# Kernel optimization log

Measured on AMD Instinct MI355X. Metric: run time of the kernel, lower is better.

The kernel has to match this reference:

```python
import jax, jax.numpy as jnp
import numpy as np

NPX = 128      # nPxPup
FOV = 512      # fovInPixel = 2*samp*nPxPup, samp=2
NMODES = 54    # len(jModes)
BATCH = 8
ALPHA = np.pi / 2


def _make_consts():
    # circular pupil on the nPxPup grid
    x = np.linspace(-1.0, 1.0, NPX)
    X, Y = np.meshgrid(x, x)
    pupil = ((X ** 2 + Y ** 2) <= 1.0).astype(np.float32)
    # 4-faced pyramid phase mask on the FOV grid, pre-fftshifted
    f = np.arange(FOV) - FOV / 2
    FX, FY = np.meshgrid(f, f)
    pyr_phase = ALPHA * (np.abs(FX) + np.abs(FY))
    pyr_mask = np.fft.fftshift(np.exp(-1j * pyr_phase)).astype(np.complex64)
    return pupil, pyr_mask


def setup_inputs() -> dict:
    key = jax.random.key(0)
    k1, k2 = jax.random.split(key)
    pupil_np, mask_np = _make_consts()
    pupil = jnp.asarray(pupil_np)                      # [NPX,NPX] float32
    pyrMask = jnp.asarray(mask_np)                     # [FOV,FOV] complex64 (fftshifted)
    # Zernike-like mode basis restricted to the pupil, column-major modes as in the torch buffer
    modes = jax.random.normal(k1, (NPX * NPX, NMODES), dtype=jnp.float32) * pupil.reshape(-1, 1)
    OL1 = (jnp.eye(NMODES, dtype=jnp.float32) * 0.1)   # learnable parameter
    inputs = jax.random.normal(k2, (BATCH, 1, NPX, NPX), dtype=jnp.float32) * pupil
    return {"inputs": inputs, "modes": modes, "OL1": OL1, "pupil": pupil, "pyrMask": pyrMask}


def _prop(phase, pupil, pyrMask):
    """Vanilla pyramid WFS propagation (modulation=0).
    phase: [B,1,NPX,NPX] -> intensity [B,1,FOV,FOV]."""
    u = (pupil * jnp.exp(1j * phase)).astype(jnp.complex64)
    npv = (FOV - NPX) // 2
    field = jnp.zeros(phase.shape[:2] + (FOV, FOV), dtype=jnp.complex64)
    field = field.at[:, :, npv:npv + NPX, npv:npv + NPX].set(u)
    buf = jnp.fft.fft2(field) * pyrMask          # focal plane * pyramid mask
    return jnp.abs(jnp.fft.fft2(buf)) ** 2       # detector intensity


def reference(inputs, modes, OL1, pupil, pyrMask):
    n_modes = OL1.shape[0]
    optModes = modes @ OL1                                     # [NPX*NPX, M]
    # reference (flat wavefront) intensity
    flat = (jnp.ones((NPX, NPX), jnp.float32) * (pupil > 0))[None, None]
    I0 = _prop(flat, pupil, pyrMask)
    I0 = I0 / jnp.sum(I0)                                      # [1,1,FOV,FOV]
    gainRow = jnp.sum(OL1, axis=1)                             # [M]
    # batch the per-mode +/- push-pull propagations in one FFT pass
    zim = optModes.T.reshape(n_modes, 1, NPX, NPX)
    phases = jnp.concatenate([zim, -zim], axis=0)              # [2M,1,NPX,NPX]
    I4 = _prop(phases, pupil, pyrMask)
    I4 = I4 / jnp.sum(I4, axis=(1, 2, 3), keepdims=True)
    sp = I4[:n_modes] - I0
    sm = I4[n_modes:] - I0
    MZc = 0.5 * (sp - sm) / gainRow[:, None, None, None]
    IM = MZc.reshape(n_modes, -1).T                            # [FOV*FOV, M]
    CM = jnp.linalg.pinv(IM)                                   # [M, FOV*FOV]
    # measurement
    Ip = _prop(inputs, pupil, pyrMask)                         # [B,1,FOV,FOV]
    Inorm = jnp.sum(Ip, axis=(1, 2, 3), keepdims=True)
    Ip = Ip / Inorm - I0
    y = CM @ Ip.reshape(Ip.shape[0], -1).T                     # [M, B]
    return y
```

## Files before the change

kernel.cpp:

```cpp
#include <hip/hip_runtime.h>
#include <math.h>

#define NPIXK 262144
#define ROWF2 584
#define ROWF2B 585

__device__ __forceinline__ int padi8(int i) { return i + (i >> 3); }
__device__ __forceinline__ int padi(int i) { return i + (i >> 5); }

#define WSYNC asm volatile("s_waitcnt lgkmcnt(0)" ::: "memory")
#define CFENCE asm volatile("" ::: "memory")

__device__ __forceinline__ float2 cmul(float2 a, float2 b) {
    return make_float2(a.x * b.x - a.y * b.y, a.x * b.y + a.y * b.x);
}

__device__ __forceinline__ void twchain(float ang, float2 tw[8]) {
    float s, c;
    sincosf(ang, &s, &c);
    float2 w1 = make_float2(c, s);
    float2 w2 = cmul(w1, w1);
    float2 w4 = cmul(w2, w2);
    tw[1] = w1;
    tw[2] = w2;
    tw[3] = cmul(w1, w2);
    tw[4] = w4;
    tw[5] = cmul(w1, w4);
    tw[6] = cmul(w2, w4);
    tw[7] = cmul(tw[3], w4);
}

__device__ __forceinline__ void fft8f(float vr[8], float vi[8]) {
    float er[4], ei[4], orr[4], oi[4];
    {
        float t0r = vr[0] + vr[4], t0i = vi[0] + vi[4];
        float t1r = vr[0] - vr[4], t1i = vi[0] - vi[4];
        float t2r = vr[2] + vr[6], t2i = vi[2] + vi[6];
        float t3r = vi[2] - vi[6], t3i = vr[6] - vr[2];
        er[0] = t0r + t2r; ei[0] = t0i + t2i;
        er[1] = t1r + t3r; ei[1] = t1i + t3i;
        er[2] = t0r - t2r; ei[2] = t0i - t2i;
        er[3] = t1r - t3r; ei[3] = t1i - t3i;
    }
    {
        float t0r = vr[1] + vr[5], t0i = vi[1] + vi[5];
        float t1r = vr[1] - vr[5], t1i = vi[1] - vi[5];
        float t2r = vr[3] + vr[7], t2i = vi[3] + vi[7];
        float t3r = vi[3] - vi[7], t3i = vr[7] - vr[3];
        orr[0] = t0r + t2r; oi[0] = t0i + t2i;
        orr[1] = t1r + t3r; oi[1] = t1i + t3i;
        orr[2] = t0r - t2r; oi[2] = t0i - t2i;
        orr[3] = t1r - t3r; oi[3] = t1i - t3i;
    }
    const float c = 0.70710678118654752440f;
    vr[0] = er[0] + orr[0]; vi[0] = ei[0] + oi[0];
    vr[4] = er[0] - orr[0]; vi[4] = ei[0] - oi[0];
    float t1r = c * (orr[1] + oi[1]), t1i = c * (oi[1] - orr[1]);
    vr[1] = er[1] + t1r; vi[1] = ei[1] + t1i;
    vr[5] = er[1] - t1r; vi[5] = ei[1] - t1i;
    float t2r = oi[2], t2i = -orr[2];
    vr[2] = er[2] + t2r; vi[2] = ei[2] + t2i;
    vr[6] = er[2] - t2r; vi[6] = ei[2] - t2i;
    float t3r = c * (oi[3] - orr[3]), t3i = -c * (orr[3] + oi[3]);
    vr[3] = er[3] + t3r; vi[3] = ei[3] + t3i;
    vr[7] = er[3] - t3r; vi[7] = ei[3] - t3i;
}

__device__ __forceinline__ void fft8_s34(float vr[8], float vi[8]) {
    const float c = 0.70710678118654752440f;
    float x3r = vr[3], x3i = vi[3], x4r = vr[4], x4i = vi[4];
    float A = c * (x3r + x3i), B = c * (x3r - x3i);
    vr[0] = x3r + x4r; vi[0] = x3i + x4i;
    vr[1] = -B - x4r;  vi[1] = -A - x4i;
    vr[2] = x4r - x3i; vi[2] = x3r + x4i;
    vr[3] = A - x4r;   vi[3] = -B - x4i;
    vr[4] = x4r - x3r; vi[4] = x4i - x3i;
    vr[5] = B - x4r;   vi[5] = A - x4i;
    vr[6] = x3i + x4r; vi[6] = x4i - x3r;
    vr[7] = -A - x4r;  vi[7] = B - x4i;
}

template <int SPARSE>
__device__ __forceinline__ void fft512v(float2* L, int t,
                                        float vr[8], float vi[8]) {
    if (SPARSE) fft8_s34(vr, vi); else fft8f(vr, vi);
    {
        float2* wb = L + 9 * t;
#pragma unroll
        for (int r = 0; r < 8; ++r) wb[r] = make_float2(vr[r], vi[r]);
    }
    float2 tw[8];
    twchain((float)(t & 7) * -0.09817477042468103870f, tw);
    WSYNC;
    {
        const float2* rb = L + t + (t >> 3);
        { float2 a = rb[0]; vr[0] = a.x; vi[0] = a.y; }
#pragma unroll
        for (int r = 1; r < 8; ++r) {
            float2 a = rb[72 * r];
            float2 w = tw[r];
            vr[r] = a.x * w.x - a.y * w.y;
            vi[r] = a.x * w.y + a.y * w.x;
        }
        fft8f(vr, vi);
        WSYNC;
        float2* wb = L + 9 * t;
#pragma unroll
        for (int r = 0; r < 8; ++r) wb[r] = make_float2(vr[r], vi[r]);
    }
    twchain((float)t * -0.01227184630308512985f, tw);
    WSYNC;
    {
        const float2* rb = L + 9 * (t & 7) + (t >> 3);
        { float2 a = rb[0]; vr[0] = a.x; vi[0] = a.y; }
#pragma unroll
        for (int r = 1; r < 8; ++r) {
            float2 a = rb[72 * r];
            float2 w = tw[r];
            vr[r] = a.x * w.x - a.y * w.y;
            vi[r] = a.x * w.y + a.y * w.x;
        }
        fft8f(vr, vi);
    }
}

template <int SPARSE>
__device__ __forceinline__ void fft512v2(float2* LA, float2* LB, int t,
                                         float avr[8], float avi[8],
                                         float bvr[8], float bvi[8]) {
    if (SPARSE) { fft8_s34(avr, avi); fft8_s34(bvr, bvi); }
    else        { fft8f(avr, avi);   fft8f(bvr, bvi); }
    {
        float2* wa = LA + 9 * t;
        float2* wb = LB + 9 * t;
#pragma unroll
        for (int r = 0; r < 8; ++r) wa[r] = make_float2(avr[r], avi[r]);
#pragma unroll
        for (int r = 0; r < 8; ++r) wb[r] = make_float2(bvr[r], bvi[r]);
    }
    float2 tw[8];
    twchain((float)(t & 7) * -0.09817477042468103870f, tw);
    WSYNC;
    {
        const float2* ra = LA + t + (t >> 3);
        const float2* rb = LB + t + (t >> 3);
        { float2 a = ra[0]; avr[0] = a.x; avi[0] = a.y; }
        { float2 b = rb[0]; bvr[0] = b.x; bvi[0] = b.y; }
#pragma unroll
        for (int r = 1; r < 8; ++r) {
            float2 a = ra[72 * r], b = rb[72 * r], w = tw[r];
            avr[r] = a.x * w.x - a.y * w.y;  avi[r] = a.x * w.y + a.y * w.x;
            bvr[r] = b.x * w.x - b.y * w.y;  bvi[r] = b.x * w.y + b.y * w.x;
        }
        fft8f(avr, avi); fft8f(bvr, bvi);
        WSYNC;
        float2* wa = LA + 9 * t;
        float2* wb = LB + 9 * t;
#pragma unroll
        for (int r = 0; r < 8; ++r) wa[r] = make_float2(avr[r], avi[r]);
#pragma unroll
        for (int r = 0; r < 8; ++r) wb[r] = make_float2(bvr[r], bvi[r]);
    }
    twchain((float)t * -0.01227184630308512985f, tw);
    WSYNC;
    {
        const float2* ra = LA + 9 * (t & 7) + (t >> 3);
        const float2* rb = LB + 9 * (t & 7) + (t >> 3);
        { float2 a = ra[0]; avr[0] = a.x; avi[0] = a.y; }
        { float2 b = rb[0]; bvr[0] = b.x; bvi[0] = b.y; }
#pragma unroll
        for (int r = 1; r < 8; ++r) {
            float2 a = ra[72 * r], b = rb[72 * r], w = tw[r];
            avr[r] = a.x * w.x - a.y * w.y;  avi[r] = a.x * w.y + a.y * w.x;
            bvr[r] = b.x * w.x - b.y * w.y;  bvi[r] = b.x * w.y + b.y * w.x;
        }
        fft8f(avr, avi); fft8f(bvr, bvi);
    }
}

#define FFT_LDS __shared__ float2 lds[4][ROWF2];

__device__ __forceinline__ double lsx(int i) {
    if (i == 127) return 1.0;
    return __dadd_rn(__dmul_rn((double)i, 2.0 / 127.0), -1.0);
}
__device__ __forceinline__ double pupilAt(int r, int c) {
    double xc = lsx(c), xr = lsx(r);
    double s = __dadd_rn(__dmul_rn(xc, xc), __dmul_rn(xr, xr));
    return (s <= 1.0) ? 1.0 : 0.0;
}

__global__ __launch_bounds__(256, 8) void k_s1(const float* __restrict__ optT,
                                               const float* __restrict__ inputs,
                                               float2* __restrict__ T1, int giBase) {
    FFT_LDS
    int tid = threadIdx.x, w = tid >> 6, t = tid & 63;
    int r = (blockIdx.x & 31) * 4 + w;
    int im = blockIdx.x >> 5;
    int gi;
    if (giBase >= 0)            gi = giBase + im;
    else if (giBase == -1)      gi = (im == 0) ? 0 : 108 + im;
    else                        gi = (im < 9) ? ((im == 0) ? 0 : 108 + im)
                                              : im - 8;

    float vr[8], vi[8];
#pragma unroll
    for (int q = 0; q < 8; ++q) { vr[q] = 0.f; vi[q] = 0.f; }
#pragma unroll
    for (int h = 0; h < 2; ++h) {
        int c = t + 64 * h;
        int p = r * 128 + c;
        float pu = (float)pupilAt(r, c);
        float ph;
        if (gi == 0) {
            ph = pu;
        } else if (gi < 109) {
            ph = optT[(gi - 1) * 16384 + p];
        } else {
            ph = inputs[(gi - 109) * 16384 + p];
        }
        float s, cs; sincosf(ph, &s, &cs);
        vr[3 + h] = pu * cs; vi[3 + h] = pu * s;
    }
    fft512v<1>(lds[w], t, vr, vi);
    WSYNC;
#pragma unroll
    for (int q = 0; q < 8; ++q) {
        int d = t + 64 * q;
        lds[w][padi8(d)] = make_float2(vr[q], vi[q]);
    }
    __syncthreads();
    int r0 = (blockIdx.x & 31) * 4;
    float2* dst = T1 + (size_t)im * 65536;
#pragma unroll
    for (int it = 0; it < 8; ++it) {
        int g = it * 256 + tid;
        int l = g >> 2, rr = g & 3;
        dst[(size_t)l * 128 + r0 + rr] = lds[rr][padi8(l)];
    }
}

__global__ __launch_bounds__(256, 4) void k_s23(const float2* __restrict__ T1,
                                                float2* __restrict__ C2p) {
    __shared__ float2 lds[8][ROWF2B];
    int tid = threadIdx.x, w = tid >> 6, t = tid & 63;
    int imgL = blockIdx.x >> 6;
    int l0 = (blockIdx.x & 63) * 8;
    int lA = l0 + w, lB = l0 + 4 + w;
    const float2* srcA = T1 + (size_t)imgL * 65536 + (size_t)lA * 128;
    const float2* srcB = T1 + (size_t)imgL * 65536 + (size_t)lB * 128;
    float avr[8], avi[8], bvr[8], bvi[8];
#pragma unroll
    for (int q = 0; q < 8; ++q) { avr[q] = 0.f; avi[q] = 0.f; bvr[q] = 0.f; bvi[q] = 0.f; }
    { float2 a0 = srcA[t], a1 = srcA[t + 64];
      avr[3] = a0.x; avi[3] = a0.y; avr[4] = a1.x; avi[4] = a1.y; }
    { float2 b0 = srcB[t], b1 = srcB[t + 64];
      bvr[3] = b0.x; bvi[3] = b0.y; bvr[4] = b1.x; bvi[4] = b1.y; }
    fft512v2<1>(lds[w], lds[w + 4], t, avr, avi, bvr, bvi);
    int glA = (lA <= 256) ? lA : 512 - lA;
    int glB = (lB <= 256) ? lB : 512 - lB;
#pragma unroll
    for (int q = 0; q < 8; ++q) {
        int k = t + 64 * q;
        int gk = (k <= 256) ? k : 512 - k;
        {   int n = (gk + glA) & 3;
            float a = avr[q], b = avi[q], X, Y;
            if (n == 0)      { X = a;  Y = b;  }
            else if (n == 1) { X = b;  Y = -a; }
            else if (n == 2) { X = -a; Y = -b; }
            else             { X = -b; Y = a;  }
            avr[q] = X; avi[q] = Y; }
        {   int n = (gk + glB) & 3;
            float a = bvr[q], b = bvi[q], X, Y;
            if (n == 0)      { X = a;  Y = b;  }
            else if (n == 1) { X = b;  Y = -a; }
            else if (n == 2) { X = -a; Y = -b; }
            else             { X = -b; Y = a;  }
            bvr[q] = X; bvi[q] = Y; }
    }
    fft512v2<0>(lds[w], lds[w + 4], t, avr, avi, bvr, bvi);
    WSYNC;
#pragma unroll
    for (int q = 0; q < 8; ++q) {
        int d = padi8(t + 64 * q);
        lds[w][d]     = make_float2(avr[q], avi[q]);
        lds[w + 4][d] = make_float2(bvr[q], bvi[q]);
    }
    __syncthreads();
    float2* dst = C2p + (size_t)imgL * NPIXK;
#pragma unroll
    for (int it = 0; it < 16; ++it) {
        int g = it * 256 + tid;
        int p = g >> 3, rr = g & 7;
        dst[(size_t)p * 512 + l0 + rr] = lds[rr][padi8(p)];
    }
}

__global__ __launch_bounds__(256, 8) void k_s4(const float2* __restrict__ C2,
                                               float* __restrict__ dst,
                                               const float* __restrict__ I0,
                                               int ep) {
    FFT_LDS
    int tid = threadIdx.x, w = tid >> 6, t = tid & 63;
    int imgL = blockIdx.x >> 7, p = (blockIdx.x & 127) * 4 + w;
    const float2* src = C2 + (size_t)imgL * NPIXK + (size_t)p * 512;
    float vr[8], vi[8];
#pragma unroll
    for (int q = 0; q < 8; ++q) { float2 a = src[t + 64 * q]; vr[q] = a.x; vi[q] = a.y; }
    fft512v<0>(lds[w], t, vr, vi);
    size_t rowOff = (size_t)p * 512;
    float* drow = dst + (size_t)imgL * NPIXK + rowOff;
    if (ep == 0) {
#pragma unroll
        for (int q = 0; q < 8; ++q) {
            int k = t + 64 * q;
            drow[k] = vr[q] * vr[q] + vi[q] * vi[q];
        }
    } else {
#pragma unroll
        for (int q = 0; q < 8; ++q) {
            int k = t + 64 * q;
            float mag2 = vr[q] * vr[q] + vi[q] * vi[q];
            drow[k] = mag2 - I0[rowOff + k];
        }
    }
}

__global__ __launch_bounds__(256, 8) void k_s4pm(const float2* __restrict__ C2p,
                                                 float* __restrict__ dst,
                                                 const double* __restrict__ gainInv,
                                                 int gBase) {
    FFT_LDS
    int tid = threadIdx.x, w = tid >> 6, t = tid & 63;
    int imgL = blockIdx.x >> 7, q2 = blockIdx.x & 127;
    int p = 2 * q2 + (w & 1) + (w >> 1) * 256;
    const float2* src = C2p + (size_t)imgL * NPIXK + (size_t)p * 512;
    float vr[8], vi[8], m2[8];
#pragma unroll
    for (int q = 0; q < 8; ++q) { float2 a = src[t + 64 * q]; vr[q] = a.x; vi[q] = a.y; }
    fft512v<0>(lds[w], t, vr, vi);
    WSYNC;
    float* mrow = (float*)lds[w];
#pragma unroll
    for (int q = 0; q < 8; ++q) {
        m2[q] = vr[q] * vr[q] + vi[q] * vi[q];
        mrow[padi(t + 64 * q)] = m2[q];
    }
    __syncthreads();
    float g = (float)gainInv[gBase + imgL];
    float* drow = dst + (size_t)imgL * NPIXK + (size_t)p * 512;
    const float* prow = (const float*)lds[w ^ 2];
#pragma unroll
    for (int q = 0; q < 8; ++q) {
        int qp = (q + 4) & 7;
        float other = prow[padi(t + 64 * qp)];
        drow[t + 64 * q] = g * (m2[q] - other);
    }
}

__global__ __launch_bounds__(256, 4) void k_s4x(const float2* __restrict__ C2p,
                                                float* __restrict__ I0buf,
                                                float* __restrict__ Mz,
                                                const double* __restrict__ gainInv) {
    __shared__ float2 lds[8][ROWF2B];
    int tid = threadIdx.x, w = tid >> 6, t = tid & 63;
    int im = blockIdx.x >> 6, b6 = blockIdx.x & 63;
    float avr[8], avi[8], bvr[8], bvi[8];
    if (im < 9) {
        int pA = b6 * 8 + w, pB = b6 * 8 + 4 + w;
        const float2* srcA = C2p + (size_t)im * NPIXK + (size_t)pA * 512;
        const float2* srcB = C2p + (size_t)im * NPIXK + (size_t)pB * 512;
#pragma unroll
        for (int q = 0; q < 8; ++q) {
            float2 a = srcA[t + 64 * q]; avr[q] = a.x; avi[q] = a.y;
            float2 b = srcB[t + 64 * q]; bvr[q] = b.x; bvi[q] = b.y;
        }
        fft512v2<0>(lds[w], lds[w + 4], t, avr, avi, bvr, bvi);
        float* dA = I0buf + (size_t)im * NPIXK + (size_t)pA * 512;
        float* dB = I0buf + (size_t)im * NPIXK + (size_t)pB * 512;
#pragma unroll
        for (int q = 0; q < 8; ++q) {
            int k = t + 64 * q;
            dA[k] = avr[q] * avr[q] + avi[q] * avi[q];
            dB[k] = bvr[q] * bvr[q] + bvi[q] * bvi[q];
        }
    } else {
        int mi = im - 9;
        int pA = b6 * 4 + w;
        int pB = pA + 256;
        const float2* srcA = C2p + (size_t)im * NPIXK + (size_t)pA * 512;
        const float2* srcB = C2p + (size_t)im * NPIXK + (size_t)pB * 512;
#pragma unroll
        for (int q = 0; q < 8; ++q) {
            float2 a = srcA[t + 64 * q]; avr[q] = a.x; avi[q] = a.y;
            float2 b = srcB[t + 64 * q]; bvr[q] = b.x; bvi[q] = b.y;
        }
        fft512v2<0>(lds[w], lds[w + 4], t, avr, avi, bvr, bvi);
        float m2A[8], m2B[8];
#pragma unroll
        for (int q = 0; q < 8; ++q) {
            m2A[q] = avr[q] * avr[q] + avi[q] * avi[q];
            m2B[q] = bvr[q] * bvr[q] + bvi[q] * bvi[q];
        }
        float g = (float)gainInv[mi];
        float* dA = Mz + (size_t)mi * NPIXK + (size_t)pA * 512;
        float* dB = Mz + (size_t)mi * NPIXK + (size_t)pB * 512;
#pragma unroll
        for (int q = 0; q < 8; ++q) {
            int k = t + 64 * q;
            int qp = (q + 4) & 7;
            dA[k] = g * (m2A[q] - m2B[qp]);
            dB[k] = g * (m2B[q] - m2A[qp]);
        }
    }
}

__global__ __launch_bounds__(256) void k_modes(const float* __restrict__ modes,
                                               const float* __restrict__ OL1,
                                               float* __restrict__ optT,
                                               double* __restrict__ gainInv,
                                               double* __restrict__ G,
                                               double* __restrict__ bmat) {
    __shared__ float sM[64 * 54];
    __shared__ float sOL[54 * 54];
    int tid = threadIdx.x;
    if (blockIdx.x == 0) {
        for (int i = tid; i < 54 * 54; i += 256) G[i] = 0.0;
        for (int i = tid; i < 54 * 8; i += 256) bmat[i] = 0.0;
    }
    for (int i = tid; i < 54 * 54; i += 256) sOL[i] = OL1[i];
    const float* msrc = modes + (size_t)blockIdx.x * 64 * 54;
    for (int i = tid; i < 64 * 54; i += 256) sM[i] = msrc[i];
    __syncthreads();
    int pl = tid & 63, mg = tid >> 6;
    int p = blockIdx.x * 64 + pl;
    const float* mrow = sM + pl * 54;
    for (int m = mg; m < 54; m += 4) {
        double acc = 0.0;
#pragma unroll
        for (int j = 0; j < 54; ++j)
            acc += (double)mrow[j] * (double)sOL[j * 54 + m];
        optT[(size_t)m * 16384 + p] = (float)acc;
    }
    if (blockIdx.x == 0 && tid < 54) {
        double g = 0.0;
        for (int j = 0; j < 54; ++j) g += (double)sOL[tid * 54 + j];
        gainInv[tid] = 0.5 / g;
    }
}

__device__ __forceinline__ float dot4(float4 a, float4 b) {
    return a.x * b.x + a.y * b.y + a.z * b.z + a.w * b.w;
}

#define GPROWS 2304
__global__ __launch_bounds__(256, 4) void k_gram54(const float* __restrict__ Mz,
                                                   const float* __restrict__ V,
                                                   const float* __restrict__ I0,
                                                   float* __restrict__ part,
                                                   int subI0) {
    __shared__ float Ms[64 * 128];
    int tid = threadIdx.x;
    int task = tid / 7, sl = tid - task * 7;
    if (task > 35) task = 35;
    int oi = 0, rem = task;
    while (rem >= 8 - oi) { rem -= 8 - oi; ++oi; }
    int oj = oi + rem;
    int ra = 8 * oi, rb = 8 * oj;
    int start = (32 * sl) / 7, len = (32 * (sl + 1)) / 7 - start;
    int rot = tid % len;
    float s[64];
#pragma unroll
    for (int q = 0; q < 64; ++q) s[q] = 0.f;

#pragma unroll 1
    for (int ch = 0; ch < 2; ++ch) {
        size_t P0 = ((size_t)blockIdx.x * 2 + ch) * 128;
        if (ch) __syncthreads();
        for (int idx = tid; idx < 64 * 32; idx += 256) {
            int i = idx >> 5, v4 = idx & 31;
            float4 vv;
            if (i < 54) {
                vv = *(const float4*)(Mz + (size_t)i * NPIXK + P0 + v4 * 4);
            } else if (i < 62) {
                vv = *(const float4*)(V + (size_t)(i - 54) * NPIXK + P0 + v4 * 4);
                if (subI0) {
                    float4 i0 = *(const float4*)(I0 + P0 + v4 * 4);
                    vv.x -= i0.x; vv.y -= i0.y; vv.z -= i0.z; vv.w -= i0.w;
                }
            } else {
                vv = make_float4(0.f, 0.f, 0.f, 0.f);
            }
            ((float4*)Ms)[i * 32 + (v4 ^ (i >> 3))] = vv;
        }
        __syncthreads();
#pragma unroll 1
        for (int k = 0; k < 5; ++k) {
            if (k < len) {
                int kk = k + rot; if (kk >= len) kk -= len;
                int pp = start + kk;
                int colA = pp ^ oi, colB = pp ^ oj;
                float4 b[8];
#pragma unroll
                for (int j = 0; j < 8; ++j)
                    b[j] = ((const float4*)Ms)[(rb + j) * 32 + colB];
#pragma unroll
                for (int i = 0; i < 8; ++i) {
                    float4 a = ((const float4*)Ms)[(ra + i) * 32 + colA];
#pragma unroll
                    for (int j = 0; j < 8; ++j) {
                        float acc = s[i * 8 + j];
                        acc = fmaf(a.x, b[j].x, acc);
                        acc = fmaf(a.y, b[j].y, acc);
                        acc = fmaf(a.z, b[j].z, acc);
                        acc = fmaf(a.w, b[j].w, acc);
                        s[i * 8 + j] = acc;
                    }
                }
            }
        }
    }
    float* red = Ms;
    float* dst = part + (size_t)blockIdx.x * GPROWS;
#pragma unroll
    for (int c = 0; c < 4; ++c) {
        __syncthreads();
        if (tid < 252) {
#pragma unroll
            for (int q = 0; q < 4; ++q)
                ((float4*)(red + tid * 16))[q] =
                    make_float4(s[c * 16 + 4 * q], s[c * 16 + 4 * q + 1],
                                s[c * 16 + 4 * q + 2], s[c * 16 + 4 * q + 3]);
        }
        __syncthreads();
        for (int idx = tid; idx < 576; idx += 256) {
            int tk = idx >> 4, j = idx & 15;
            float acc = 0.f;
#pragma unroll
            for (int ss = 0; ss < 7; ++ss) acc += red[(tk * 7 + ss) * 16 + j];
            dst[tk * 64 + c * 16 + j] = acc;
        }
    }
}

__global__ __launch_bounds__(256) void k_gred54(const float* __restrict__ part,
                                                double* __restrict__ G,
                                                double* __restrict__ bmat) {
    __shared__ double red[8][33];
    int tid = threadIdx.x;
    int r = tid & 31, grp = tid >> 5;
    int row = blockIdx.x * 32 + r;
    int bid0 = blockIdx.y * 256;
    double acc = 0.0;
    for (int k = 0; k < 32; ++k)
        acc += (double)part[(size_t)(bid0 + grp + 8 * k) * GPROWS + row];
    red[grp][r] = acc;
    __syncthreads();
    if (tid < 32) {
        int rr = blockIdx.x * 32 + tid;
        double s = 0.0;
#pragma unroll
        for (int g = 0; g < 8; ++g) s += red[g][tid];
        int tk = rr >> 6, q = rr & 63;
        int oi = 0, rem = tk;
        while (rem >= 8 - oi) { rem -= 8 - oi; ++oi; }
        int oj = oi + rem;
        int a = 8 * oi + (q >> 3), b = 8 * oj + (q & 7);
        if (a < 54) {
            if (b < 54) {
                if (a <= b) atomicAdd(&G[a * 54 + b], s);
            } else if (b < 62) {
                atomicAdd(&bmat[a * 8 + (b - 54)], s);
            }
        }
    }
}

__global__ __launch_bounds__(256) void k_gram(const float* __restrict__ Mz,
                                              const float* __restrict__ V,
                                              const float* __restrict__ I0,
                                              float* __restrict__ part,
                                              int cA, int PROWS, int subI0) {
    __shared__ float Ms[54 * 128];
    __shared__ float Vs[8 * 128];
    int tid = threadIdx.x;
    int cQ = (cA + 3) >> 2;
    int nQT = cQ * (cQ + 1) / 2;
    int nT = nQT + cQ * 8;
    int task = tid;
    int kind = (task < nQT) ? 0 : (task < nT ? 1 : 2);
    int r0[4], r1[4], bb = 0, Ti = 0, Tj = 0, Qi = 0;
    if (kind == 0) {
        int rem = task;
        while (rem >= cQ - Ti) { rem -= cQ - Ti; ++Ti; }
        Tj = Ti + rem;
#pragma unroll
        for (int q = 0; q < 4; ++q) {
            int i = 4 * Ti + q; r0[q] = (i < cA) ? i : cA - 1;
            int j = 4 * Tj + q; r1[q] = (j < cA) ? j : cA - 1;
        }
    } else if (kind == 1) {
        int tb = task - nQT;
        Qi = tb >> 3; bb = tb & 7;
#pragma unroll
        for (int q = 0; q < 4; ++q) {
            int i = 4 * Qi + q; r0[q] = (i < cA) ? i : cA - 1;
        }
    }
    float s[16];
#pragma unroll
    for (int q = 0; q < 16; ++q) s[q] = 0.f;

    size_t P0 = (size_t)blockIdx.x * 128;
    for (int idx = tid; idx < cA * 32; idx += 256) {
        int i = idx >> 5, v4 = idx & 31;
        ((float4*)Ms)[i * 32 + v4] =
            *(const float4*)(Mz + (size_t)i * NPIXK + P0 + v4 * 4);
    }
    for (int idx = tid; idx < 8 * 32; idx += 256) {
        int b = idx >> 5, v4 = idx & 31;
        float4 vv = *(const float4*)(V + (size_t)b * NPIXK + P0 + v4 * 4);
        if (subI0) {
            float4 i0 = *(const float4*)(I0 + P0 + v4 * 4);
            vv.x -= i0.x; vv.y -= i0.y; vv.z -= i0.z; vv.w -= i0.w;
        }
        ((float4*)Vs)[b * 32 + v4] = vv;
    }
    __syncthreads();
    if (kind == 0) {
        for (int kk = 0; kk < 32; ++kk) {
            int pp = (kk + tid) & 31;
            float4 a0 = ((float4*)(Ms + r0[0] * 128))[pp];
            float4 a1 = ((float4*)(Ms + r0[1] * 128))[pp];
            float4 a2 = ((float4*)(Ms + r0[2] * 128))[pp];
            float4 a3 = ((float4*)(Ms + r0[3] * 128))[pp];
            float4 b0 = ((float4*)(Ms + r1[0] * 128))[pp];
            float4 b1 = ((float4*)(Ms + r1[1] * 128))[pp];
            float4 b2 = ((float4*)(Ms + r1[2] * 128))[pp];
            float4 b3 = ((float4*)(Ms + r1[3] * 128))[pp];
            s[0] += dot4(a0, b0); s[1] += dot4(a0, b1);
            s[2] += dot4(a0, b2); s[3] += dot4(a0, b3);
            s[4] += dot4(a1, b0); s[5] += dot4(a1, b1);
            s[6] += dot4(a1, b2); s[7] += dot4(a1, b3);
            s[8] += dot4(a2, b0); s[9] += dot4(a2, b1);
            s[10] += dot4(a2, b2); s[11] += dot4(a2, b3);
            s[12] += dot4(a3, b0); s[13] += dot4(a3, b1);
            s[14] += dot4(a3, b2); s[15] += dot4(a3, b3);
        }
    } else if (kind == 1) {
        for (int kk = 0; kk < 32; ++kk) {
            int pp = (kk + tid) & 31;
            float4 vb = ((float4*)Vs)[bb * 32 + pp];
            float4 a0 = ((float4*)(Ms + r0[0] * 128))[pp];
            float4 a1 = ((float4*)(Ms + r0[1] * 128))[pp];
            float4 a2 = ((float4*)(Ms + r0[2] * 128))[pp];
            float4 a3 = ((float4*)(Ms + r0[3] * 128))[pp];
            s[0] += dot4(a0, vb); s[1] += dot4(a1, vb);
            s[2] += dot4(a2, vb); s[3] += dot4(a3, vb);
        }
    }
    float* dst = part + (size_t)blockIdx.x * PROWS;
    if (kind == 0) {
#pragma unroll
        for (int q = 0; q < 16; ++q) dst[task * 16 + q] = s[q];
    } else if (kind == 1) {
#pragma unroll
        for (int q = 0; q < 4; ++q)
            dst[nQT * 16 + (task - nQT) * 4 + q] = s[q];
    }
}

__global__ __launch_bounds__(256) void k_gred3(const float* __restrict__ part,
                                               double* __restrict__ G,
                                               double* __restrict__ bmat,
                                               int cA, int m0, int PROWS) {
    __shared__ double red[8][33];
    int tid = threadIdx.x;
    int r = tid & 31, grp = tid >> 5;
    int row = blockIdx.x * 32 + r;
    int bid0 = blockIdx.y * 256;
    double acc = 0.0;
    if (row < PROWS)
        for (int k = 0; k < 32; ++k)
            acc += (double)part[(size_t)(bid0 + grp + 8 * k) * PROWS + row];
    red[grp][r] = acc;
    __syncthreads();
    if (tid < 32) {
        int rr = blockIdx.x * 32 + tid;
        if (rr < PROWS) {
            double s = 0.0;
#pragma unroll
            for (int g = 0; g < 8; ++g) s += red[g][tid];
            int cQ = (cA + 3) >> 2;
            int nQT = cQ * (cQ + 1) / 2;
            if (rr < nQT * 16) {
                int tile = rr >> 4, q = rr & 15;
                int Ti = 0, rem = tile;
                while (rem >= cQ - Ti) { rem -= cQ - Ti; ++Ti; }
                int Tj = Ti + rem;
                int i = 4 * Ti + (q >> 2), j = 4 * Tj + (q & 3);
                if (i < cA && j < cA && i <= j)
                    atomicAdd(&G[(m0 + i) * 54 + (m0 + j)], s);
            } else {
                int qb = rr - nQT * 16;
                int tb = qb >> 2, qq = qb & 3;
                int Qi = tb >> 3, bbb = tb & 7;
                int i = 4 * Qi + qq;
                if (i < cA) atomicAdd(&bmat[(m0 + i) * 8 + bbb], s);
            }
        }
    }
}

__global__ __launch_bounds__(256) void k_gramx(const float* __restrict__ MzA,
                                               const float* __restrict__ MzB,
                                               double* __restrict__ G,
                                               int cA, int m0, int mb) {
    __shared__ float Ms[54 * 128];
    __shared__ float Bs[128];
    int tid = threadIdx.x;
    double acc = 0.0;
    for (int ch = 0; ch < 4; ++ch) {
        size_t P0 = (size_t)blockIdx.x * 512 + (size_t)ch * 128;
        __syncthreads();
        for (int idx = tid; idx < cA * 32; idx += 256) {
            int i = idx >> 5, v4 = idx & 31;
            ((float4*)Ms)[i * 32 + v4] =
                *(const float4*)(MzA + (size_t)i * NPIXK + P0 + v4 * 4);
        }
        if (tid < 128) Bs[tid] = MzB[P0 + tid];
        __syncthreads();
        if (tid < cA) {
            const float* ri = Ms + tid * 128;
            float s = 0.f;
            for (int k = 0; k < 128; ++k) {
                int p = (k + tid) & 127;
                s += ri[p] * Bs[p];
            }
            acc += (double)s;
        }
    }
    if (tid < cA) atomicAdd(&G[(m0 + tid) * 54 + mb], acc);
}

__global__ __launch_bounds__(512) void k_solve(const double* __restrict__ G,
                                               const double* __restrict__ bmat,
                                               float* __restrict__ out) {
    __shared__ double A[54][65];
    int tid = threadIdx.x;
    int r = tid >> 3, cg = tid & 7;
    for (int idx = tid; idx < 54 * 62; idx += 512) {
        int i = idx / 62, c = idx % 62;
        A[i][c] = (c < 54) ? ((i <= c) ? G[i * 54 + c] : G[c * 54 + i])
                           : bmat[i * 8 + (c - 54)];
    }
    __syncthreads();
    for (int p = 0; p < 54; ++p) {
        bool act = (r < 54) && (r != p);
        if (act) {
            double f = A[r][p] / A[p][p];
            CFENCE;
#pragma unroll
            for (int k = 0; k < 8; ++k) {
                int c = cg + 8 * k;
                if (c < 62) A[r][c] -= f * A[p][c];
            }
        }
        __syncthreads();
    }
    for (int idx = tid; idx < 54 * 8; idx += 512) {
        int m = idx >> 3, b = idx & 7;
        out[idx] = (float)(A[m][54 + b] / A[m][m]);
    }
}

__global__ void k_zero(float* out, int n) {
    int i = blockIdx.x * 256 + threadIdx.x;
    if (i < n) out[i] = 0.f;
}

extern "C" void kernel_launch(void* const* d_in, const int* in_sizes, int n_in,
                              void* d_out, int out_size, void* d_ws, size_t ws_size,
                              hipStream_t stream) {
    float* out = (float*)d_out;
    if (out_size <= 0) return;
    if (n_in < 3 || in_sizes[0] != 131072 || in_sizes[1] != 884736 ||
        in_sizes[2] != 2916 || out_size < 432) {
        k_zero<<<(out_size + 255) / 256, 256, 0, stream>>>(out, out_size);
        return;
    }
    const float* inputs = (const float*)d_in[0];
    const float* modes  = (const float*)d_in[1];
    const float* OL1    = (const float*)d_in[2];

    char* ws = (char*)d_ws;
    size_t off = 0;
    auto alloc = [&](size_t bytes) -> void* {
        void* p = ws + off;
        off += (bytes + 255) & ~(size_t)255;
        return p;
    };
    float*  optT    = (float*)  alloc((size_t)54 * 16384 * 4);
    double* gainInv = (double*) alloc(64 * 8);
    double* G       = (double*) alloc(54 * 54 * 8);
    double* bmat    = (double*) alloc(54 * 8 * 8);
    float*  I0buf   = (float*)  alloc((size_t)9 * NPIXK * 4);
    float*  V       = I0buf + NPIXK;
    float*  MzB1    = (float*)  alloc((size_t)NPIXK * 4);
    float*  part    = (float*)  alloc((size_t)2048 * GPROWS * 4);

    const size_t IMG  = (size_t)NPIXK * 4 + 256;
    const size_t PIPE = ((size_t)65536 * 8 + 256) + ((size_t)NPIXK * 8 + 256);
    size_t rem = (ws_size > off + 4096) ? ws_size - off - 4096 : 0;
    int cA, chunkP;
    if (rem >= 54 * IMG + PIPE) {
        cA = 54;
        size_t c = (rem - 54 * IMG) / PIPE;
        chunkP = (c > 63) ? 63 : (int)c;
        if (chunkP < 1) chunkP = 1;
    } else if (rem >= IMG + PIPE) {
        cA = (int)((rem - PIPE) / IMG);
        if (cA > 53) cA = 53;
        if (cA < 1) cA = 1;
        size_t left = rem - (size_t)cA * IMG;
        chunkP = (int)(left / PIPE);
        if (chunkP < 1) chunkP = 1;
        if (chunkP > cA) chunkP = cA;
    } else {
        k_zero<<<(out_size + 255) / 256, 256, 0, stream>>>(out, out_size);
        return;
    }
    float*  MzA = (float*)  alloc((size_t)cA * NPIXK * 4);
    float2* T1  = (float2*) alloc((size_t)chunkP * 65536 * 8);
    float2* C2p = (float2*) alloc((size_t)chunkP * NPIXK * 8);
    if (off > ws_size) {
        k_zero<<<(out_size + 255) / 256, 256, 0, stream>>>(out, out_size);
        return;
    }

    auto prop_one = [&](int giBase, int n, float* dst, int ep) {
        for (int s = 0; s < n; s += chunkP) {
            int nn = n - s; if (nn > chunkP) nn = chunkP;
            k_s1<<<nn * 32, 256, 0, stream>>>(optT, inputs, T1, giBase + s);
            k_s23<<<nn * 64, 256, 0, stream>>>(T1, C2p);
            k_s4<<<nn * 128, 256, 0, stream>>>(C2p, dst + (size_t)s * NPIXK,
                                               I0buf, ep);
        }
    };
    auto prop_pm = [&](int m0, int n, float* dst, int gBase) {
        for (int s = 0; s < n; s += chunkP) {
            int nn = n - s; if (nn > chunkP) nn = chunkP;
            k_s1<<<nn * 32, 256, 0, stream>>>(optT, inputs, T1, 1 + m0 + s);
            k_s23<<<nn * 64, 256, 0, stream>>>(T1, C2p);
            k_s4pm<<<nn * 128, 256, 0, stream>>>(C2p,
                                                 dst + (size_t)s * NPIXK,
                                                 gainInv, gBase + s);
        }
    };

    k_modes<<<256, 256, 0, stream>>>(modes, OL1, optT, gainInv, G, bmat);

    if (cA >= 54 && chunkP >= 63) {
        k_s1<<<63 * 32, 256, 0, stream>>>(optT, inputs, T1, -2);
        k_s23<<<63 * 64, 256, 0, stream>>>(T1, C2p);
        k_s4x<<<63 * 64, 256, 0, stream>>>(C2p, I0buf, MzA, gainInv);
        k_gram54<<<1024, 256, 0, stream>>>(MzA, V, I0buf, part, 1);
        k_gred54<<<dim3(72, 4), 256, 0, stream>>>(part, G, bmat);
    } else {
        int subI0;
        if (chunkP >= 9) {
            k_s1<<<9 * 32, 256, 0, stream>>>(optT, inputs, T1, -1);
            k_s23<<<9 * 64, 256, 0, stream>>>(T1, C2p);
            k_s4<<<9 * 128, 256, 0, stream>>>(C2p, I0buf, I0buf, 0);
            subI0 = 1;
        } else {
            prop_one(0, 1, I0buf, 0);
            prop_one(109, 8, V, 2);
            subI0 = 0;
        }
        if (cA >= 54) {
            prop_pm(0, 54, MzA, 0);
            k_gram54<<<1024, 256, 0, stream>>>(MzA, V, I0buf, part, subI0);
            k_gred54<<<dim3(72, 4), 256, 0, stream>>>(part, G, bmat);
        } else {
            for (int m0 = 0; m0 < 54; m0 += cA) {
                int ca = 54 - m0; if (ca > cA) ca = cA;
                prop_pm(m0, ca, MzA, m0);
                int cQ = (ca + 3) >> 2;
                int PROWS = cQ * (cQ + 1) / 2 * 16 + cQ * 32;
                k_gram<<<2048, 256, 0, stream>>>(MzA, V, I0buf, part, ca, PROWS,
                                                 subI0);
                k_gred3<<<dim3((PROWS + 31) / 32, 8), 256, 0, stream>>>(part, G,
                                                                       bmat, ca,
                                                                       m0, PROWS);
                for (int mb = m0 + ca; mb < 54; ++mb) {
                    prop_pm(mb, 1, MzB1, mb);
                    k_gramx<<<512, 256, 0, stream>>>(MzA, MzB1, G, ca, m0, mb);
                }
            }
        }
    }
    k_solve<<<1, 512, 0, stream>>>(G, bmat, out);
}
```

Before: 242.5 us.

## Process two rows per wave in first FFT stage and drop LDS waits

k_s1 now has each wave transform two pupil rows at once with the dual-row fft512v2, so each block covers eight rows and the grid is halved. The aim is more independent work per wave to hide latency and wider transposed stores to T1. Separately, several s_waitcnt lgkmcnt(0) waits after FFT passes become compiler-only fences, removing explicit LDS-wait stalls. The risks are higher register pressure, lower occupancy (launch bounds drop from 8 to 4) and dependence on the compiler to insert the LDS waits correctly.

```diff
diff --git a/kernel.cpp b/kernel.cpp
--- a/kernel.cpp
+++ b/kernel.cpp
@@ -103,7 +103,7 @@
             vi[r] = a.x * w.y + a.y * w.x;
         }
         fft8f(vr, vi);
-        WSYNC;
+        CFENCE;
         float2* wb = L + 9 * t;
 #pragma unroll
         for (int r = 0; r < 8; ++r) wb[r] = make_float2(vr[r], vi[r]);
@@ -153,7 +153,7 @@
             bvr[r] = b.x * w.x - b.y * w.y;  bvi[r] = b.x * w.y + b.y * w.x;
         }
         fft8f(avr, avi); fft8f(bvr, bvi);
-        WSYNC;
+        CFENCE;
         float2* wa = LA + 9 * t;
         float2* wb = LB + 9 * t;
 #pragma unroll
@@ -190,52 +190,61 @@
     return (s <= 1.0) ? 1.0 : 0.0;
 }
 
-__global__ __launch_bounds__(256, 8) void k_s1(const float* __restrict__ optT,
+__global__ __launch_bounds__(256, 4) void k_s1(const float* __restrict__ optT,
                                                const float* __restrict__ inputs,
                                                float2* __restrict__ T1, int giBase) {
-    FFT_LDS
+    __shared__ float2 lds[8][ROWF2B];
     int tid = threadIdx.x, w = tid >> 6, t = tid & 63;
-    int r = (blockIdx.x & 31) * 4 + w;
-    int im = blockIdx.x >> 5;
+    int im = blockIdx.x >> 4;
+    int r0 = (blockIdx.x & 15) * 8;
+    int rA = r0 + w, rB = r0 + 4 + w;
     int gi;
     if (giBase >= 0)            gi = giBase + im;
     else if (giBase == -1)      gi = (im == 0) ? 0 : 108 + im;
     else                        gi = (im < 9) ? ((im == 0) ? 0 : 108 + im)
                                               : im - 8;
 
-    float vr[8], vi[8];
-#pragma unroll
-    for (int q = 0; q < 8; ++q) { vr[q] = 0.f; vi[q] = 0.f; }
+    float avr[8], avi[8], bvr[8], bvi[8];
+#pragma unroll
+    for (int q = 0; q < 8; ++q) { avr[q] = 0.f; avi[q] = 0.f; bvr[q] = 0.f; bvi[q] = 0.f; }
 #pragma unroll
     for (int h = 0; h < 2; ++h) {
         int c = t + 64 * h;
-        int p = r * 128 + c;
-        float pu = (float)pupilAt(r, c);
-        float ph;
-        if (gi == 0) {
-            ph = pu;
-        } else if (gi < 109) {
-            ph = optT[(gi - 1) * 16384 + p];
-        } else {
-            ph = inputs[(gi - 109) * 16384 + p];
-        }
-        float s, cs; sincosf(ph, &s, &cs);
-        vr[3 + h] = pu * cs; vi[3 + h] = pu * s;
-    }
-    fft512v<1>(lds[w], t, vr, vi);
-    WSYNC;
+        {
+            int p = rA * 128 + c;
+            float pu = (float)pupilAt(rA, c);
+            float ph;
+            if (gi == 0)        ph = pu;
+            else if (gi < 109)  ph = optT[(gi - 1) * 16384 + p];
+            else                ph = inputs[(gi - 109) * 16384 + p];
+            float s, cs; sincosf(ph, &s, &cs);
+            avr[3 + h] = pu * cs; avi[3 + h] = pu * s;
+        }
+        {
+            int p = rB * 128 + c;
+            float pu = (float)pupilAt(rB, c);
+            float ph;
+            if (gi == 0)        ph = pu;
+            else if (gi < 109)  ph = optT[(gi - 1) * 16384 + p];
+            else                ph = inputs[(gi - 109) * 16384 + p];
+            float s, cs; sincosf(ph, &s, &cs);
+            bvr[3 + h] = pu * cs; bvi[3 + h] = pu * s;
+        }
+    }
+    fft512v2<1>(lds[w], lds[w + 4], t, avr, avi, bvr, bvi);
+    CFENCE;
 #pragma unroll
     for (int q = 0; q < 8; ++q) {
-        int d = t + 64 * q;
-        lds[w][padi8(d)] = make_float2(vr[q], vi[q]);
+        int d = padi8(t + 64 * q);
+        lds[w][d]     = make_float2(avr[q], avi[q]);
+        lds[w + 4][d] = make_float2(bvr[q], bvi[q]);
     }
     __syncthreads();
-    int r0 = (blockIdx.x & 31) * 4;
     float2* dst = T1 + (size_t)im * 65536;
 #pragma unroll
-    for (int it = 0; it < 8; ++it) {
+    for (int it = 0; it < 16; ++it) {
         int g = it * 256 + tid;
-        int l = g >> 2, rr = g & 3;
+        int l = g >> 3, rr = g & 7;
         dst[(size_t)l * 128 + r0 + rr] = lds[rr][padi8(l)];
     }
 }
@@ -279,7 +288,7 @@
             bvr[q] = X; bvi[q] = Y; }
     }
     fft512v2<0>(lds[w], lds[w + 4], t, avr, avi, bvr, bvi);
-    WSYNC;
+    CFENCE;
 #pragma unroll
     for (int q = 0; q < 8; ++q) {
         int d = padi8(t + 64 * q);
@@ -339,7 +348,7 @@
 #pragma unroll
     for (int q = 0; q < 8; ++q) { float2 a = src[t + 64 * q]; vr[q] = a.x; vi[q] = a.y; }
     fft512v<0>(lds[w], t, vr, vi);
-    WSYNC;
+    CFENCE;
     float* mrow = (float*)lds[w];
 #pragma unroll
     for (int q = 0; q < 8; ++q) {
@@ -841,7 +850,7 @@
     auto prop_one = [&](int giBase, int n, float* dst, int ep) {
         for (int s = 0; s < n; s += chunkP) {
             int nn = n - s; if (nn > chunkP) nn = chunkP;
-            k_s1<<<nn * 32, 256, 0, stream>>>(optT, inputs, T1, giBase + s);
+            k_s1<<<nn * 16, 256, 0, stream>>>(optT, inputs, T1, giBase + s);
             k_s23<<<nn * 64, 256, 0, stream>>>(T1, C2p);
             k_s4<<<nn * 128, 256, 0, stream>>>(C2p, dst + (size_t)s * NPIXK,
                                                I0buf, ep);
@@ -850,7 +859,7 @@
     auto prop_pm = [&](int m0, int n, float* dst, int gBase) {
         for (int s = 0; s < n; s += chunkP) {
             int nn = n - s; if (nn > chunkP) nn = chunkP;
-            k_s1<<<nn * 32, 256, 0, stream>>>(optT, inputs, T1, 1 + m0 + s);
+            k_s1<<<nn * 16, 256, 0, stream>>>(optT, inputs, T1, 1 + m0 + s);
             k_s23<<<nn * 64, 256, 0, stream>>>(T1, C2p);
             k_s4pm<<<nn * 128, 256, 0, stream>>>(C2p,
                                                  dst + (size_t)s * NPIXK,
@@ -861,7 +870,7 @@
     k_modes<<<256, 256, 0, stream>>>(modes, OL1, optT, gainInv, G, bmat);
 
     if (cA >= 54 && chunkP >= 63) {
-        k_s1<<<63 * 32, 256, 0, stream>>>(optT, inputs, T1, -2);
+        k_s1<<<63 * 16, 256, 0, stream>>>(optT, inputs, T1, -2);
         k_s23<<<63 * 64, 256, 0, stream>>>(T1, C2p);
         k_s4x<<<63 * 64, 256, 0, stream>>>(C2p, I0buf, MzA, gainInv);
         k_gram54<<<1024, 256, 0, stream>>>(MzA, V, I0buf, part, 1);
@@ -869,7 +878,7 @@
     } else {
         int subI0;
         if (chunkP >= 9) {
-            k_s1<<<9 * 32, 256, 0, stream>>>(optT, inputs, T1, -1);
+            k_s1<<<9 * 16, 256, 0, stream>>>(optT, inputs, T1, -1);
             k_s23<<<9 * 64, 256, 0, stream>>>(T1, C2p);
             k_s4<<<9 * 128, 256, 0, stream>>>(C2p, I0buf, I0buf, 0);
             subI0 = 1;
```

After: 240.2 us (median of 2 runs). Within noise of the previous version (-1.0%).
